# Performance work log

Hardware: AMD Instinct MI355X
Metric: run time of the kernel (lower is better)

The kernel has to match this reference:

```python
import jax, jax.numpy as jnp
import numpy as np

T, B, E, H = 2048, 2, 2048, 16
D = E // H  # 128


def setup_inputs() -> dict:
    key = jax.random.key(0)
    ks = jax.random.split(key, 4)
    query = jax.random.normal(ks[0], (T, B, E), dtype=jnp.float32)
    Wqkv = jax.random.normal(ks[1], (3 * E, E), dtype=jnp.float32) * 0.02
    bqkv = jnp.zeros((3 * E,), dtype=jnp.float32)
    Wo = jax.random.normal(ks[2], (E, E), dtype=jnp.float32) * 0.02
    bo = jnp.zeros((E,), dtype=jnp.float32)
    # Llama rotary frequencies: freqs_cis[t, j] = exp(i * t * theta^{-2j/D})
    inv_freq = 1.0 / (10000.0 ** (np.arange(0, D, 2, dtype=np.float32) / D))  # (D/2,)
    angles = np.arange(T, dtype=np.float32)[:, None] * inv_freq[None, :]       # (T, D/2)
    freqs_cos = jnp.asarray(np.cos(angles), dtype=jnp.float32)
    freqs_sin = jnp.asarray(np.sin(angles), dtype=jnp.float32)
    return {"query": query, "Wqkv": Wqkv, "bqkv": bqkv, "Wo": Wo, "bo": bo,
            "freqs_cos": freqs_cos, "freqs_sin": freqs_sin}


def _apply_rope(x, cos, sin):
    # Faithful to metaseq: x is (T, B, E) but view()-ed as (B, T, H, D);
    # jnp.reshape is the same row-major reinterpretation as torch .view().
    xr = x.reshape(B, T, H, D // 2, 2)
    x0, x1 = xr[..., 0], xr[..., 1]
    c = cos[None, :, None, :]  # broadcast over batch and heads, seq_dim=1
    s = sin[None, :, None, :]
    o0 = x0 * c - x1 * s
    o1 = x0 * s + x1 * c
    return jnp.stack([o0, o1], axis=-1).reshape(T, B, E)


def reference(query, Wqkv, bqkv, Wo, bo, freqs_cos, freqs_sin):
    # Combined QKV projection (ColumnParallelLinear, world_size=1), split order (k, v, q)
    kvq = jnp.einsum('tbe,fe->tbf', query, Wqkv) + bqkv  # (T, B, 3E)
    k, v, q = jnp.split(kvq, 3, axis=-1)
    q = _apply_rope(q, freqs_cos, freqs_sin)
    k = _apply_rope(k, freqs_cos, freqs_sin)
    # scaling split as sqrt(head_dim^-0.5) on both q and k (baddbmm path)
    s = jnp.asarray(D, jnp.float32) ** -0.25
    qb = q.reshape(T, B * H, D).swapaxes(0, 1) * s   # (BH, T, D)
    kb = k.reshape(T, B * H, D).swapaxes(0, 1) * s   # (BH, S, D)
    vb = v.reshape(T, B * H, D).swapaxes(0, 1)       # (BH, S, D)
    scores = jnp.einsum('btd,bsd->bts', qb, kb)      # (BH, T, S)
    causal = jnp.tril(jnp.ones((T, T), dtype=bool))  # ScaledUpperTriangMaskedSoftmax
    scores = jnp.where(causal[None, :, :], scores, jnp.finfo(scores.dtype).min)
    probs = jax.nn.softmax(scores, axis=-1)          # dropout p=0 -> identity
    attn = jnp.einsum('bts,bsd->btd', probs, vb)     # (BH, T, D)
    attn = attn.swapaxes(0, 1).reshape(T, B, E)
    # RowParallelLinear with skip_bias_add=True: bias returned separately (not added)
    out = jnp.einsum('tbe,fe->tbf', attn, Wo)
    return out
```

## Files before the change

### kernel.cpp

```cpp
#include <hip/hip_runtime.h>
#include <stdint.h>

typedef unsigned short u16;
typedef __attribute__((ext_vector_type(4))) float f32x4;
typedef __attribute__((ext_vector_type(8))) short bf16x8;
typedef __attribute__((ext_vector_type(8))) u16 u16x8;

#define T_SEQ  2048
#define EMB    2048
#define HD     128
#define NHEAD  16
#define NTOK   4096
#define NE3    6144
#define SCALE  0.29730177875068026f
#define LOG2E  1.44269504088896f

typedef __attribute__((address_space(3))) char* lds_t;
typedef const __attribute__((address_space(1))) char* gl_t;

__device__ __forceinline__ void gld16(const void* g, void* l) {
  __builtin_amdgcn_global_load_lds((gl_t)g, (lds_t)l, 16, 0, 0);
}

__device__ __forceinline__ u16 f2bf(float f) {
  union { float f; uint32_t u; } c; c.f = f;
  uint32_t r = c.u + 0x7fffu + ((c.u >> 16) & 1u);
  return (u16)(r >> 16);
}

__global__ __launch_bounds__(256) void cvt_bf16(const float* __restrict__ in,
                                                u16* __restrict__ out, int n8) {
  int i = blockIdx.x * 256 + threadIdx.x;
  if (i >= n8) return;
  const float4* p = (const float4*)in + (size_t)i * 2;
  float4 a = p[0], b = p[1];
  u16x8 o;
  o[0]=f2bf(a.x); o[1]=f2bf(a.y); o[2]=f2bf(a.z); o[3]=f2bf(a.w);
  o[4]=f2bf(b.x); o[5]=f2bf(b.y); o[6]=f2bf(b.z); o[7]=f2bf(b.w);
  *((u16x8*)out + i) = o;
}

template<int EPI>
__global__ __launch_bounds__(256, 2) void gemm_bt(
    const u16* __restrict__ A, const u16* __restrict__ Bm, int K, int N,
    const float* __restrict__ cosT, const float* __restrict__ sinT,
    const float* __restrict__ bias,
    u16* __restrict__ Qh, u16* __restrict__ Kh, u16* __restrict__ Vt,
    float* __restrict__ Cout)
{
  __shared__ u16 As[128*32];
  __shared__ u16 Bs[128*32];
  const int tid = threadIdx.x;
  const int lane = tid & 63, w = tid >> 6;
  const int wm = w >> 1, wn = w & 1;
  const int l15 = lane & 15, lq = lane >> 4;
  const int bM = blockIdx.x, bN = blockIdx.y;

  const u16* Ab = A + (size_t)bM * 128 * K;
  const u16* Bb = Bm + (size_t)bN * 128 * K;
  const int r0 = tid >> 2;
  const int c0 = (tid & 3) * 8;

  f32x4 acc[4][4] = {};

  for (int kt = 0; kt < K; kt += 32) {
    gld16(Ab + (size_t)r0        * K + kt + c0, (char*)As + tid*16);
    gld16(Ab + (size_t)(r0 + 64) * K + kt + c0, (char*)As + tid*16 + 4096);
    gld16(Bb + (size_t)r0        * K + kt + c0, (char*)Bs + tid*16);
    gld16(Bb + (size_t)(r0 + 64) * K + kt + c0, (char*)Bs + tid*16 + 4096);
    __syncthreads();
    bf16x8 af[4], bfr[4];
    #pragma unroll
    for (int i = 0; i < 4; i++)
      af[i] = *(const bf16x8*)(As + (wm*64 + i*16 + l15)*32 + lq*8);
    #pragma unroll
    for (int i = 0; i < 4; i++)
      bfr[i] = *(const bf16x8*)(Bs + (wn*64 + i*16 + l15)*32 + lq*8);
    #pragma unroll
    for (int mi = 0; mi < 4; mi++)
      #pragma unroll
      for (int ni = 0; ni < 4; ni++)
        acc[mi][ni] = __builtin_amdgcn_mfma_f32_16x16x32_bf16(af[mi], bfr[ni], acc[mi][ni], 0, 0, 0);
    __syncthreads();
  }

  if (EPI == 0) {
    #pragma unroll
    for (int mi = 0; mi < 4; mi++) {
      int row = bM*128 + wm*64 + mi*16 + lq*4;
      #pragma unroll
      for (int ni = 0; ni < 4; ni++) {
        int col = bN*128 + wn*64 + ni*16 + l15;
        #pragma unroll
        for (int r = 0; r < 4; r++)
          Cout[(size_t)(row + r) * N + col] = acc[mi][ni][r];
      }
    }
  } else {
    const int cbase = bN*128 + wn*64;
    const int seg  = cbase >> 11;
    const int head = (cbase >> 7) & 15;
    #pragma unroll
    for (int mi = 0; mi < 4; mi++) {
      #pragma unroll
      for (int ni = 0; ni < 4; ni++) {
        int col = cbase + ni*16 + l15;
        int d = col & 127;
        float bi = bias[col];
        f32x4 v = acc[mi][ni];
        #pragma unroll
        for (int r = 0; r < 4; r++) {
          int n = bM*128 + wm*64 + mi*16 + lq*4 + r;
          float val = v[r] + bi;
          int t = n >> 1, b = n & 1;
          int bh = b*NHEAD + head;
          if (seg == 1) {
            Vt[((size_t)bh*HD + d)*T_SEQ + t] = f2bf(val);
          } else {
            float par = __shfl_xor(val, 1);
            int fidx = d >> 1;
            float cs = cosT[(n & (T_SEQ-1))*64 + fidx];
            float sn = sinT[(n & (T_SEQ-1))*64 + fidx];
            val = (d & 1) ? (par*sn + val*cs) : (val*cs - par*sn);
            val *= SCALE;
            u16* dst = (seg == 0) ? Kh : Qh;
            dst[((size_t)bh*T_SEQ + t)*HD + d] = f2bf(val);
          }
        }
      }
    }
  }
}

__global__ __launch_bounds__(256, 4) void attn_fwd(
    const u16* __restrict__ Qh, const u16* __restrict__ Kh,
    const u16* __restrict__ Vt, u16* __restrict__ O)
{
  const int i = blockIdx.x;
  const int kk = i >> 8, c = i & 255;
  const int bh = (c >> 5) + kk * 8;
  const int b5 = c & 31;
  const int qb = (kk & 1) ? (31 - b5) : b5;

  const int tid = threadIdx.x, lane = tid & 63, w = tid >> 6;
  const int l15 = lane & 15, lq = lane >> 4;

  __shared__ u16 Ks[64*128];
  __shared__ u16 Vs[128*64];
  __shared__ char Ps[4][2048];

  const int q0 = qb*64 + w*16;
  bf16x8 qf[4];
  #pragma unroll
  for (int dc = 0; dc < 4; dc++)
    qf[dc] = *(const bf16x8*)(Qh + ((size_t)bh*T_SEQ + q0 + l15)*HD + dc*32 + lq*8);

  f32x4 o[8] = {};
  float m[4], l_[4];
  #pragma unroll
  for (int r = 0; r < 4; r++) { m[r] = -1e30f; l_[r] = 0.f; }

  const int nkb = qb + 1;
  for (int kb = 0; kb < nkb; ++kb) {
    #pragma unroll
    for (int j = 0; j < 4; j++) {
      int lb = tid*16 + j*4096;
      int row = lb >> 8, bir = lb & 255;
      int sb = bir ^ ((row & 7) << 4);
      gld16((const char*)Kh + (((size_t)bh*T_SEQ + kb*64 + row) << 8) + sb,
            (char*)Ks + lb);
    }
    #pragma unroll
    for (int j = 0; j < 4; j++) {
      int lb = tid*16 + j*4096;
      int row = lb >> 7, bir = lb & 127;
      int sb = bir ^ ((row & 7) << 4);
      gld16((const char*)Vt + ((size_t)(bh*HD + row)*T_SEQ)*2 + kb*128 + sb,
            (char*)Vs + lb);
    }
    __syncthreads();

    f32x4 sacc[4];
    #pragma unroll
    for (int nf = 0; nf < 4; nf++) {
      f32x4 z = {};
      sacc[nf] = z;
      #pragma unroll
      for (int dc = 0; dc < 4; dc++) {
        int row = nf*16 + l15;
        int bir = (dc*64 + lq*16) ^ ((row & 7) << 4);
        bf16x8 kf = *(const bf16x8*)((const char*)Ks + row*256 + bir);
        sacc[nf] = __builtin_amdgcn_mfma_f32_16x16x32_bf16(qf[dc], kf, sacc[nf], 0, 0, 0);
      }
    }

    if (kb == qb) {
      #pragma unroll
      for (int nf = 0; nf < 4; nf++)
        #pragma unroll
        for (int r = 0; r < 4; r++) {
          int key = kb*64 + nf*16 + l15;
          int qr  = q0 + lq*4 + r;
          if (key > qr) sacc[nf][r] = -1e30f;
        }
    }

    #pragma unroll
    for (int r = 0; r < 4; r++) {
      float mx = fmaxf(fmaxf(sacc[0][r], sacc[1][r]), fmaxf(sacc[2][r], sacc[3][r]));
      mx = fmaxf(mx, __shfl_xor(mx, 1));
      mx = fmaxf(mx, __shfl_xor(mx, 2));
      mx = fmaxf(mx, __shfl_xor(mx, 4));
      mx = fmaxf(mx, __shfl_xor(mx, 8));
      float newm = fmaxf(m[r], mx);
      float scale = exp2f((m[r] - newm) * LOG2E);
      float sum = 0.f;
      #pragma unroll
      for (int nf = 0; nf < 4; nf++) {
        float p = exp2f((sacc[nf][r] - newm) * LOG2E);
        sacc[nf][r] = p;
        sum += p;
      }
      sum += __shfl_xor(sum, 1);
      sum += __shfl_xor(sum, 2);
      sum += __shfl_xor(sum, 4);
      sum += __shfl_xor(sum, 8);
      l_[r] = l_[r] * scale + sum;
      m[r] = newm;
      #pragma unroll
      for (int nf = 0; nf < 8; nf++) o[nf][r] *= scale;
    }

    #pragma unroll
    for (int nf = 0; nf < 4; nf++)
      #pragma unroll
      for (int r = 0; r < 4; r++) {
        int prow = lq*4 + r;
        int pbyte = prow*128 + ((((nf*16 + l15)*2)) ^ ((prow & 7) << 4));
        *(u16*)(Ps[w] + pbyte) = f2bf(sacc[nf][r]);
      }

    #pragma unroll
    for (int kc = 0; kc < 2; kc++) {
      int pb = (kc*64 + lq*16) ^ ((l15 & 7) << 4);
      bf16x8 pf = *(const bf16x8*)(Ps[w] + l15*128 + pb);
      #pragma unroll
      for (int nf = 0; nf < 8; nf++) {
        int row = nf*16 + l15;
        int bir = (kc*64 + lq*16) ^ ((row & 7) << 4);
        bf16x8 vf = *(const bf16x8*)((const char*)Vs + row*128 + bir);
        o[nf] = __builtin_amdgcn_mfma_f32_16x16x32_bf16(pf, vf, o[nf], 0, 0, 0);
      }
    }
    __syncthreads();
  }

  const int b = bh >> 4, h = bh & 15;
  #pragma unroll
  for (int r = 0; r < 4; r++) {
    float inv = 1.0f / l_[r];
    int t = q0 + lq*4 + r;
    size_t base = ((size_t)(t*2 + b))*EMB + h*HD;
    #pragma unroll
    for (int nf = 0; nf < 8; nf++)
      O[base + nf*16 + l15] = f2bf(o[nf][r] * inv);
  }
}

extern "C" void kernel_launch(void* const* d_in, const int* in_sizes, int n_in,
                              void* d_out, int out_size, void* d_ws, size_t ws_size,
                              hipStream_t stream) {
  const float* query = (const float*)d_in[0];
  const float* Wqkv  = (const float*)d_in[1];
  const float* bqkv  = (const float*)d_in[2];
  const float* Wo    = (const float*)d_in[3];
  const float* fcos  = (const float*)d_in[5];
  const float* fsin  = (const float*)d_in[6];
  float* out = (float*)d_out;
  char* ws = (char*)d_ws;

  u16* WQb = (u16*)(ws + 0);
  u16* WOb = (u16*)(ws + 25165824);
  u16* A1  = (u16*)(ws + 33554432);
  u16* QH  = (u16*)(ws + 50331648);
  u16* KH  = (u16*)(ws + 67108864);
  u16* VT  = (u16*)(ws + 83886080);

  cvt_bf16<<<4096, 256, 0, stream>>>(query, A1, 1048576);
  cvt_bf16<<<6144, 256, 0, stream>>>(Wqkv, WQb, 1572864);
  cvt_bf16<<<2048, 256, 0, stream>>>(Wo,   WOb,  524288);

  gemm_bt<1><<<dim3(32, 48), 256, 0, stream>>>(A1, WQb, 2048, NE3,
                                               fcos, fsin, bqkv, QH, KH, VT, nullptr);

  attn_fwd<<<1024, 256, 0, stream>>>(QH, KH, VT, A1);

  gemm_bt<0><<<dim3(32, 16), 256, 0, stream>>>(A1, WOb, 2048, EMB,
                                               nullptr, nullptr, nullptr,
                                               nullptr, nullptr, nullptr, out);
}
```

Before: 360.7 us.

## Replace bf16 GEMMs with 256x256-tile double-buffered swizzled LDS pipeline kernel

Both projection GEMMs move from a 128x128, single-buffered, K=32 kernel to a 512-thread kernel with 256x256 tiles and K=64 steps. The new kernel double-buffers LDS (128 KB) and uses an XOR swizzle against bank conflicts. Async global-to-LDS loads for the next tile are interleaved between MFMA groups, gated by waitcnt/barrier macros, with s_setprio around the math and a remapped block index for L2 locality. The aim is to hide load latency, cut barrier overhead and raise reuse per loaded byte. The cost is fewer, larger blocks: 384 for QKV and only 128 for the output projection, which may leave many CUs idle and limits occupancy to one block per CU.

Result: no change. 359.4 us (-0.4%).

```diff
diff --git a/kernel.cpp b/kernel.cpp
--- a/kernel.cpp
+++ b/kernel.cpp
@@ -26,6 +26,24 @@
   union { float f; uint32_t u; } c; c.f = f;
   uint32_t r = c.u + 0x7fffu + ((c.u >> 16) & 1u);
   return (u16)(r >> 16);
+}
+
+#define GATE(N) do { \
+  asm volatile("s_waitcnt vmcnt(" #N ")" ::: "memory"); \
+  __builtin_amdgcn_s_barrier(); \
+  __builtin_amdgcn_sched_barrier(0); \
+} while (0)
+
+__device__ __forceinline__ bf16x8 ldsrd(const char* base, int row, int ks, int lq) {
+  return *(const bf16x8*)(base + row*128 + ((ks*64 + lq*16) ^ ((row & 7) << 4)));
+}
+
+__device__ __forceinline__ void stage(const char* g, int rowstride, int ktb,
+                                      char* l, int j, int tid) {
+  int lb = j*8192 + tid*16;
+  int row = lb >> 7;
+  int src = (lb & 127) ^ ((row & 7) << 4);
+  gld16(g + (size_t)row*rowstride + ktb + src, l + lb);
 }
 
 __global__ __launch_bounds__(256) void cvt_bf16(const float* __restrict__ in,
@@ -40,68 +58,120 @@
   *((u16x8*)out + i) = o;
 }
 
-template<int EPI>
-__global__ __launch_bounds__(256, 2) void gemm_bt(
+template<int EPI, int NBN>
+__global__ __launch_bounds__(512, 2) void gemm8(
     const u16* __restrict__ A, const u16* __restrict__ Bm, int K, int N,
     const float* __restrict__ cosT, const float* __restrict__ sinT,
     const float* __restrict__ bias,
     u16* __restrict__ Qh, u16* __restrict__ Kh, u16* __restrict__ Vt,
     float* __restrict__ Cout)
 {
-  __shared__ u16 As[128*32];
-  __shared__ u16 Bs[128*32];
+  __shared__ __align__(16) char lds[131072];
   const int tid = threadIdx.x;
   const int lane = tid & 63, w = tid >> 6;
-  const int wm = w >> 1, wn = w & 1;
+  const int wm = w >> 2, wn = w & 3;
   const int l15 = lane & 15, lq = lane >> 4;
-  const int bM = blockIdx.x, bN = blockIdx.y;
-
-  const u16* Ab = A + (size_t)bM * 128 * K;
-  const u16* Bb = Bm + (size_t)bN * 128 * K;
-  const int r0 = tid >> 2;
-  const int c0 = (tid & 3) * 8;
-
-  f32x4 acc[4][4] = {};
-
-  for (int kt = 0; kt < K; kt += 32) {
-    gld16(Ab + (size_t)r0        * K + kt + c0, (char*)As + tid*16);
-    gld16(Ab + (size_t)(r0 + 64) * K + kt + c0, (char*)As + tid*16 + 4096);
-    gld16(Bb + (size_t)r0        * K + kt + c0, (char*)Bs + tid*16);
-    gld16(Bb + (size_t)(r0 + 64) * K + kt + c0, (char*)Bs + tid*16 + 4096);
-    __syncthreads();
-    bf16x8 af[4], bfr[4];
-    #pragma unroll
-    for (int i = 0; i < 4; i++)
-      af[i] = *(const bf16x8*)(As + (wm*64 + i*16 + l15)*32 + lq*8);
-    #pragma unroll
-    for (int i = 0; i < 4; i++)
-      bfr[i] = *(const bf16x8*)(Bs + (wn*64 + i*16 + l15)*32 + lq*8);
+
+  const int q8 = gridDim.x >> 3;
+  const int swz = (blockIdx.x & 7) * q8 + (blockIdx.x >> 3);
+  const int bM = swz / NBN, bN = swz % NBN;
+
+  const char* Ag = (const char*)(A + (size_t)bM * 256 * K);
+  const char* Bg = (const char*)(Bm + (size_t)bN * 256 * K);
+  const int K2 = K * 2;
+  const int nT = K >> 6;
+
+  stage(Bg, K2, 0, lds + 32768, 0, tid);
+  stage(Bg, K2, 0, lds + 32768, 1, tid);
+  stage(Bg, K2, 0, lds + 32768, 2, tid);
+  stage(Bg, K2, 0, lds + 32768, 3, tid);
+  stage(Ag, K2, 0, lds, 0, tid);
+  stage(Ag, K2, 0, lds, 2, tid);
+  stage(Ag, K2, 0, lds, 1, tid);
+  stage(Ag, K2, 0, lds, 3, tid);
+
+  f32x4 acc[8][4] = {};
+
+  for (int t = 0; t < nT; ++t) {
+    const char* Al = lds + (t & 1) * 65536;
+    const char* Bl = Al + 32768;
+    char* Asn = lds + ((t + 1) & 1) * 65536;
+    char* Bsn = Asn + 32768;
+    const int ktb = (t + 1 < nT ? t + 1 : t) << 7;
+
+    GATE(2);
+    bf16x8 bf0[4], bf1[4], af[4];
+    #pragma unroll
+    for (int ni = 0; ni < 4; ni++) bf0[ni] = ldsrd(Bl, wn*64 + ni*16 + l15, 0, lq);
+    #pragma unroll
+    for (int i = 0; i < 4; i++) af[i] = ldsrd(Al, wm*128 + i*16 + l15, 0, lq);
+    stage(Bg, K2, ktb, Bsn, 0, tid);
+    stage(Bg, K2, ktb, Bsn, 1, tid);
+    __builtin_amdgcn_s_setprio(1);
     #pragma unroll
     for (int mi = 0; mi < 4; mi++)
       #pragma unroll
       for (int ni = 0; ni < 4; ni++)
-        acc[mi][ni] = __builtin_amdgcn_mfma_f32_16x16x32_bf16(af[mi], bfr[ni], acc[mi][ni], 0, 0, 0);
-    __syncthreads();
+        acc[mi][ni] = __builtin_amdgcn_mfma_f32_16x16x32_bf16(af[mi], bf0[ni], acc[mi][ni], 0, 0, 0);
+    __builtin_amdgcn_s_setprio(0);
+    #pragma unroll
+    for (int ni = 0; ni < 4; ni++) bf1[ni] = ldsrd(Bl, wn*64 + ni*16 + l15, 1, lq);
+    #pragma unroll
+    for (int i = 0; i < 4; i++) af[i] = ldsrd(Al, wm*128 + i*16 + l15, 1, lq);
+    stage(Bg, K2, ktb, Bsn, 2, tid);
+    stage(Bg, K2, ktb, Bsn, 3, tid);
+    __builtin_amdgcn_s_setprio(1);
+    #pragma unroll
+    for (int mi = 0; mi < 4; mi++)
+      #pragma unroll
+      for (int ni = 0; ni < 4; ni++)
+        acc[mi][ni] = __builtin_amdgcn_mfma_f32_16x16x32_bf16(af[mi], bf1[ni], acc[mi][ni], 0, 0, 0);
+    __builtin_amdgcn_s_setprio(0);
+
+    GATE(4);
+    #pragma unroll
+    for (int i = 0; i < 4; i++) af[i] = ldsrd(Al, wm*128 + 64 + i*16 + l15, 0, lq);
+    stage(Ag, K2, ktb, Asn, 0, tid);
+    stage(Ag, K2, ktb, Asn, 2, tid);
+    __builtin_amdgcn_s_setprio(1);
+    #pragma unroll
+    for (int mi = 0; mi < 4; mi++)
+      #pragma unroll
+      for (int ni = 0; ni < 4; ni++)
+        acc[4+mi][ni] = __builtin_amdgcn_mfma_f32_16x16x32_bf16(af[mi], bf0[ni], acc[4+mi][ni], 0, 0, 0);
+    __builtin_amdgcn_s_setprio(0);
+    #pragma unroll
+    for (int i = 0; i < 4; i++) af[i] = ldsrd(Al, wm*128 + 64 + i*16 + l15, 1, lq);
+    stage(Ag, K2, ktb, Asn, 1, tid);
+    stage(Ag, K2, ktb, Asn, 3, tid);
+    __builtin_amdgcn_s_setprio(1);
+    #pragma unroll
+    for (int mi = 0; mi < 4; mi++)
+      #pragma unroll
+      for (int ni = 0; ni < 4; ni++)
+        acc[4+mi][ni] = __builtin_amdgcn_mfma_f32_16x16x32_bf16(af[mi], bf1[ni], acc[4+mi][ni], 0, 0, 0);
+    __builtin_amdgcn_s_setprio(0);
   }
+  asm volatile("s_waitcnt vmcnt(0)" ::: "memory");
 
   if (EPI == 0) {
     #pragma unroll
-    for (int mi = 0; mi < 4; mi++) {
-      int row = bM*128 + wm*64 + mi*16 + lq*4;
+    for (int mi = 0; mi < 8; mi++) {
+      int row = bM*256 + wm*128 + mi*16 + lq*4;
       #pragma unroll
       for (int ni = 0; ni < 4; ni++) {
-        int col = bN*128 + wn*64 + ni*16 + l15;
+        int col = bN*256 + wn*64 + ni*16 + l15;
         #pragma unroll
         for (int r = 0; r < 4; r++)
           Cout[(size_t)(row + r) * N + col] = acc[mi][ni][r];
       }
     }
   } else {
-    const int cbase = bN*128 + wn*64;
+    const int cbase = bN*256 + wn*64;
     const int seg  = cbase >> 11;
     const int head = (cbase >> 7) & 15;
     #pragma unroll
-    for (int mi = 0; mi < 4; mi++) {
+    for (int mi = 0; mi < 8; mi++) {
       #pragma unroll
       for (int ni = 0; ni < 4; ni++) {
         int col = cbase + ni*16 + l15;
@@ -110,7 +180,7 @@
         f32x4 v = acc[mi][ni];
         #pragma unroll
         for (int r = 0; r < 4; r++) {
-          int n = bM*128 + wm*64 + mi*16 + lq*4 + r;
+          int n = bM*256 + wm*128 + mi*16 + lq*4 + r;
           float val = v[r] + bi;
           int t = n >> 1, b = n & 1;
           int bh = b*NHEAD + head;
@@ -290,12 +360,12 @@
   cvt_bf16<<<6144, 256, 0, stream>>>(Wqkv, WQb, 1572864);
   cvt_bf16<<<2048, 256, 0, stream>>>(Wo,   WOb,  524288);
 
-  gemm_bt<1><<<dim3(32, 48), 256, 0, stream>>>(A1, WQb, 2048, NE3,
-                                               fcos, fsin, bqkv, QH, KH, VT, nullptr);
+  gemm8<1, 24><<<384, 512, 0, stream>>>(A1, WQb, 2048, NE3,
+                                        fcos, fsin, bqkv, QH, KH, VT, nullptr);
 
   attn_fwd<<<1024, 256, 0, stream>>>(QH, KH, VT, A1);
 
-  gemm_bt<0><<<dim3(32, 16), 256, 0, stream>>>(A1, WOb, 2048, EMB,
-                                               nullptr, nullptr, nullptr,
-                                               nullptr, nullptr, nullptr, out);
-}
+  gemm8<0, 8><<<128, 512, 0, stream>>>(A1, WOb, 2048, EMB,
+                                       nullptr, nullptr, nullptr,
+                                       nullptr, nullptr, nullptr, out);
+}
```

## Rewrite projection GEMMs with multi-stage LDS pipeline, swizzled layout and larger tiles

Applied to the files above, without the earlier changes.

Replaces the synchronous GEMM with a 512-thread kernel that uses 128x256 tiles and a 4-slot LDS ring, so global-to-LDS loads for later k-steps are issued while MFMAs run on the current ones. LDS rows are XOR-swizzled to cut bank conflicts, the block index is remapped for L2 locality, and s_setprio raises priority around the MFMA section. The goal is to hide memory latency and remove the two barriers per k-step. In exchange it uses 96KB of LDS per block, which limits occupancy, and relies on hand-placed waitcnt and barrier ordering.

Result: faster. 350.0 us (-3.0%).

```diff
diff --git a/kernel.cpp b/kernel.cpp
--- a/kernel.cpp
+++ b/kernel.cpp
@@ -40,49 +40,94 @@
   *((u16x8*)out + i) = o;
 }
 
-template<int EPI>
-__global__ __launch_bounds__(256, 2) void gemm_bt(
+
+__device__ __forceinline__ bf16x8 rdfrag(const char* slot, int row, int lq) {
+  return *(const bf16x8*)(slot + row*64 + ((lq ^ ((row >> 1) & 3)) << 4));
+}
+__device__ __forceinline__ void stageA(const char* Ag, int K2, int ktb, int ks,
+                                       char* slot, int tid) {
+  int row = tid >> 2, c = tid & 3;
+  gld16(Ag + (size_t)row*K2 + ktb + ks*64 + ((c ^ ((row >> 1) & 3)) << 4),
+        slot + tid*16);
+}
+__device__ __forceinline__ void stageB(const char* Bg, int K2, int ktb, int ks,
+                                       char* slot, int j, int tid) {
+  int lb = j*8192 + tid*16;
+  int row = lb >> 6, c = (lb >> 4) & 3;
+  gld16(Bg + (size_t)row*K2 + ktb + ks*64 + ((c ^ ((row >> 1) & 3)) << 4),
+        slot + lb);
+}
+
+template<int EPI, int NBN>
+__global__ __launch_bounds__(512, 2) void gemmP(
     const u16* __restrict__ A, const u16* __restrict__ Bm, int K, int N,
     const float* __restrict__ cosT, const float* __restrict__ sinT,
     const float* __restrict__ bias,
     u16* __restrict__ Qh, u16* __restrict__ Kh, u16* __restrict__ Vt,
     float* __restrict__ Cout)
 {
-  __shared__ u16 As[128*32];
-  __shared__ u16 Bs[128*32];
+  __shared__ __align__(16) char lds[98304];
   const int tid = threadIdx.x;
   const int lane = tid & 63, w = tid >> 6;
-  const int wm = w >> 1, wn = w & 1;
+  const int wm = w >> 2, wn = w & 3;
   const int l15 = lane & 15, lq = lane >> 4;
-  const int bM = blockIdx.x, bN = blockIdx.y;
-
-  const u16* Ab = A + (size_t)bM * 128 * K;
-  const u16* Bb = Bm + (size_t)bN * 128 * K;
-  const int r0 = tid >> 2;
-  const int c0 = (tid & 3) * 8;
+
+  const int q8 = gridDim.x >> 3;
+  const int swz = (blockIdx.x & 7) * q8 + (blockIdx.x >> 3);
+  const int bM = swz / NBN, bN = swz % NBN;
+
+  const char* Ag = (const char*)(A + (size_t)bM * 128 * K);
+  const char* Bg = (const char*)(Bm + (size_t)bN * 256 * K);
+  const int K2 = K * 2;
+  const int nT = K >> 6;
+
+  stageA(Ag, K2, 0,   0, lds + 0,     tid);
+  stageB(Bg, K2, 0,   0, lds + 32768, 0, tid);
+  stageB(Bg, K2, 0,   0, lds + 32768, 1, tid);
+  stageA(Ag, K2, 0,   1, lds + 8192,  tid);
+  stageB(Bg, K2, 0,   1, lds + 49152, 0, tid);
+  stageB(Bg, K2, 0,   1, lds + 49152, 1, tid);
+  stageA(Ag, K2, 128, 0, lds + 16384, tid);
+  stageB(Bg, K2, 128, 0, lds + 65536, 0, tid);
+  stageB(Bg, K2, 128, 0, lds + 65536, 1, tid);
 
   f32x4 acc[4][4] = {};
 
-  for (int kt = 0; kt < K; kt += 32) {
-    gld16(Ab + (size_t)r0        * K + kt + c0, (char*)As + tid*16);
-    gld16(Ab + (size_t)(r0 + 64) * K + kt + c0, (char*)As + tid*16 + 4096);
-    gld16(Bb + (size_t)r0        * K + kt + c0, (char*)Bs + tid*16);
-    gld16(Bb + (size_t)(r0 + 64) * K + kt + c0, (char*)Bs + tid*16 + 4096);
-    __syncthreads();
-    bf16x8 af[4], bfr[4];
-    #pragma unroll
-    for (int i = 0; i < 4; i++)
-      af[i] = *(const bf16x8*)(As + (wm*64 + i*16 + l15)*32 + lq*8);
-    #pragma unroll
-    for (int i = 0; i < 4; i++)
-      bfr[i] = *(const bf16x8*)(Bs + (wn*64 + i*16 + l15)*32 + lq*8);
-    #pragma unroll
-    for (int mi = 0; mi < 4; mi++)
-      #pragma unroll
-      for (int ni = 0; ni < 4; ni++)
-        acc[mi][ni] = __builtin_amdgcn_mfma_f32_16x16x32_bf16(af[mi], bfr[ni], acc[mi][ni], 0, 0, 0);
-    __syncthreads();
+  for (int t = 0; t < nT; ++t) {
+    #pragma unroll
+    for (int ks = 0; ks < 2; ++ks) {
+      const int q = 2*t + ks;
+      const int ts = (q + 3) >> 1, kss = (q + 3) & 1;
+      const int tsc = ts < nT ? ts : nT - 1;
+      const char* Asl = lds + ((t & 1)*2 + ks)*8192;
+      const char* Bsl = lds + 32768 + ((t & 1)*2 + ks)*16384;
+      char* AslS = lds + ((ts & 1)*2 + kss)*8192;
+      char* BslS = lds + 32768 + ((ts & 1)*2 + kss)*16384;
+
+      asm volatile("s_waitcnt vmcnt(6)" ::: "memory");
+      __builtin_amdgcn_s_barrier();
+      __builtin_amdgcn_sched_barrier(0);
+
+      bf16x8 af[4], bf[4];
+      #pragma unroll
+      for (int i = 0; i < 4; i++) af[i] = rdfrag(Asl, wm*64 + i*16 + l15, lq);
+      #pragma unroll
+      for (int i = 0; i < 4; i++) bf[i] = rdfrag(Bsl, wn*64 + i*16 + l15, lq);
+      stageA(Ag, K2, tsc << 7, kss, AslS, tid);
+      stageB(Bg, K2, tsc << 7, kss, BslS, 0, tid);
+      stageB(Bg, K2, tsc << 7, kss, BslS, 1, tid);
+      asm volatile("s_waitcnt lgkmcnt(0)" ::: "memory");
+      __builtin_amdgcn_sched_barrier(0);
+      __builtin_amdgcn_s_setprio(1);
+      #pragma unroll
+      for (int mi = 0; mi < 4; mi++)
+        #pragma unroll
+        for (int ni = 0; ni < 4; ni++)
+          acc[mi][ni] = __builtin_amdgcn_mfma_f32_16x16x32_bf16(af[mi], bf[ni], acc[mi][ni], 0, 0, 0);
+      __builtin_amdgcn_s_setprio(0);
+    }
   }
+  asm volatile("s_waitcnt vmcnt(0)" ::: "memory");
 
   if (EPI == 0) {
     #pragma unroll
@@ -90,14 +135,14 @@
       int row = bM*128 + wm*64 + mi*16 + lq*4;
       #pragma unroll
       for (int ni = 0; ni < 4; ni++) {
-        int col = bN*128 + wn*64 + ni*16 + l15;
+        int col = bN*256 + wn*64 + ni*16 + l15;
         #pragma unroll
         for (int r = 0; r < 4; r++)
           Cout[(size_t)(row + r) * N + col] = acc[mi][ni][r];
       }
     }
   } else {
-    const int cbase = bN*128 + wn*64;
+    const int cbase = bN*256 + wn*64;
     const int seg  = cbase >> 11;
     const int head = (cbase >> 7) & 15;
     #pragma unroll
@@ -290,12 +335,12 @@
   cvt_bf16<<<6144, 256, 0, stream>>>(Wqkv, WQb, 1572864);
   cvt_bf16<<<2048, 256, 0, stream>>>(Wo,   WOb,  524288);
 
-  gemm_bt<1><<<dim3(32, 48), 256, 0, stream>>>(A1, WQb, 2048, NE3,
-                                               fcos, fsin, bqkv, QH, KH, VT, nullptr);
+  gemmP<1, 24><<<768, 512, 0, stream>>>(A1, WQb, 2048, NE3,
+                                        fcos, fsin, bqkv, QH, KH, VT, nullptr);
 
   attn_fwd<<<1024, 256, 0, stream>>>(QH, KH, VT, A1);
 
-  gemm_bt<0><<<dim3(32, 16), 256, 0, stream>>>(A1, WOb, 2048, EMB,
-                                               nullptr, nullptr, nullptr,
-                                               nullptr, nullptr, nullptr, out);
-}
+  gemmP<0, 8><<<256, 512, 0, stream>>>(A1, WOb, 2048, EMB,
+                                       nullptr, nullptr, nullptr,
+                                       nullptr, nullptr, nullptr, out);
+}
```
